# Kernel optimization log

Hardware: AMD Instinct MI355X
Metric: run time of the kernel (lower is better)

The kernel has to match this reference:

```python
import jax, jax.numpy as jnp
import numpy as np

N_NODES = 50000
N_EDGES = 800000
IN_DIM = 256
H1 = 512
H2 = 128


def _gcn_conv(x, W, b, row, col, ew, n_nodes):
    """PyG GCNConv with edge_weight: linear (no bias) -> add self-loops ->
    symmetric normalization -> weighted scatter-add -> + bias."""
    xw = x @ W  # [N, out]
    loop = jnp.arange(n_nodes, dtype=row.dtype)
    row_f = jnp.concatenate([row, loop])
    col_f = jnp.concatenate([col, loop])
    ew_f = jnp.concatenate([ew, jnp.ones((n_nodes,), dtype=ew.dtype)])
    deg = jax.ops.segment_sum(ew_f, col_f, num_segments=n_nodes)  # in-degree
    dinv = jnp.where(deg > 0, jax.lax.rsqrt(jnp.where(deg > 0, deg, 1.0)), 0.0)
    norm = dinv[row_f] * ew_f * dinv[col_f]  # [E+N]
    msg = norm[:, None] * xw[row_f]          # [E+N, out] gather
    out = jax.ops.segment_sum(msg, col_f, num_segments=n_nodes)  # scatter-add
    return out + b


def _prelu(x, alpha):
    return jnp.where(x >= 0, x, alpha * x)


def setup_inputs() -> dict:
    key = jax.random.key(0)
    ks = jax.random.split(key, 6)
    x = jax.random.normal(ks[0], (N_NODES, IN_DIM), dtype=jnp.float32)
    edge_index = jax.random.randint(ks[1], (2, N_EDGES), 0, N_NODES, dtype=jnp.int32)
    edge_attr = jax.random.uniform(ks[2], (N_EDGES,), dtype=jnp.float32)
    W1 = jax.random.normal(ks[3], (IN_DIM, H1), dtype=jnp.float32) / np.sqrt(IN_DIM)
    b1 = jnp.zeros((H1,), dtype=jnp.float32)
    W2 = jax.random.normal(ks[4], (H1, H2), dtype=jnp.float32) / np.sqrt(H1)
    b2 = jnp.zeros((H2,), dtype=jnp.float32)
    alpha = jnp.ones((1,), dtype=jnp.float32) * 0.25  # nn.PReLU default init
    return {"x": x, "edge_attr": edge_attr, "W1": W1, "b1": b1,
            "W2": W2, "b2": b2, "alpha": alpha, "edge_index": edge_index}


def reference(x, edge_attr, W1, b1, W2, b2, alpha, edge_index):
    row, col = edge_index[0], edge_index[1]
    # Dropout treated as identity (deterministic eval-mode reference).
    feat1 = _prelu(_gcn_conv(x, W1, b1, row, col, edge_attr, N_NODES), alpha)
    feat2 = _prelu(_gcn_conv(feat1, W2, b2, row, col, edge_attr, N_NODES), alpha)
    return feat2
```

## Files before the change

### kernel.cpp

```cpp
#include <hip/hip_runtime.h>

#define N_NODES 50000
#define N_EDGES 800000
#define IN_DIM  256
#define H1      512
#define H2      128

typedef __attribute__((ext_vector_type(8))) short  short8v;
typedef __attribute__((ext_vector_type(4))) float  float4v;
typedef __attribute__((ext_vector_type(4))) unsigned short ushort4v;

__device__ __forceinline__ void split_bf16(float v, unsigned short& h, unsigned short& l) {
    unsigned u = __builtin_bit_cast(unsigned, v);
    unsigned hr = (u + 0x7FFFu + ((u >> 16) & 1u)) >> 16;
    float hf = __builtin_bit_cast(float, hr << 16);
    float lf = v - hf;
    unsigned ul = __builtin_bit_cast(unsigned, lf);
    unsigned lr = (ul + 0x7FFFu + ((ul >> 16) & 1u)) >> 16;
    h = (unsigned short)hr; l = (unsigned short)lr;
}


__global__ void init_kernel(float* deg, int* cnt, int n) {
    int i = blockIdx.x * blockDim.x + threadIdx.x;
    if (i < n) { deg[i] = 1.0f; cnt[i] = 0; }
}

__global__ void edge_deg_kernel(const int* __restrict__ col, const float* __restrict__ ew,
                                float* deg, int* cnt, int ne) {
    int e = blockIdx.x * blockDim.x + threadIdx.x;
    if (e < ne) {
        int c = col[e];
        atomicAdd(&deg[c], ew[e]);
        atomicAdd(&cnt[c], 1);
    }
}

__global__ void dinv_kernel(const float* __restrict__ deg, float* dinv, int n) {
    int i = blockIdx.x * blockDim.x + threadIdx.x;
    if (i < n) dinv[i] = rsqrtf(deg[i]);
}

__global__ void scan_block_kernel(const int* __restrict__ cnt, int* __restrict__ part,
                                  int* __restrict__ bsum, int n) {
    __shared__ int s[256];
    int tid = threadIdx.x;
    int i = blockIdx.x * 256 + tid;
    int v = (i < n) ? cnt[i] : 0;
    s[tid] = v; __syncthreads();
#pragma unroll
    for (int d = 1; d < 256; d <<= 1) {
        int t = (tid >= d) ? s[tid - d] : 0; __syncthreads();
        s[tid] += t; __syncthreads();
    }
    if (i < n) part[i] = s[tid] - v;
    if (tid == 255) bsum[blockIdx.x] = s[255];
}

__global__ void scan_tops_kernel(const int* __restrict__ bsum, int* __restrict__ boff, int nb) {
    __shared__ int s[256];
    int tid = threadIdx.x;
    int v = (tid < nb) ? bsum[tid] : 0;
    s[tid] = v; __syncthreads();
#pragma unroll
    for (int d = 1; d < 256; d <<= 1) {
        int t = (tid >= d) ? s[tid - d] : 0; __syncthreads();
        s[tid] += t; __syncthreads();
    }
    if (tid < nb) boff[tid] = s[tid] - v;
}

__global__ void scan_add_kernel(const int* __restrict__ part, const int* __restrict__ boff,
                                int* __restrict__ ptr, int* __restrict__ fill, int n) {
    int i = blockIdx.x * 256 + threadIdx.x;
    if (i < n) {
        int p = part[i] + boff[blockIdx.x];
        ptr[i] = p; fill[i] = p;
    }
    if (i == 0) ptr[n] = N_EDGES;
}

__global__ void scatter_kernel(const int* __restrict__ row, const int* __restrict__ col,
                               const float* __restrict__ ew, const float* __restrict__ dinv,
                               int* fill, int2* __restrict__ edges, int ne) {
    int e = blockIdx.x * blockDim.x + threadIdx.x;
    if (e < ne) {
        int r = row[e], c = col[e];
        int pos = atomicAdd(&fill[c], 1);
        float w = dinv[r] * ew[e] * dinv[c];
        edges[pos] = make_int2(r, __float_as_int(w));
    }
}

__global__ void convw_kernel(const float* __restrict__ W, unsigned short* __restrict__ Wh,
                             unsigned short* __restrict__ Wl, int K, int N) {
    int idx = blockIdx.x * 256 + threadIdx.x;
    if (idx < N * K) {
        int n = idx / K, k = idx % K;
        unsigned short h, l;
        split_bf16(W[(size_t)k * N + n], h, l);
        Wh[idx] = h; Wl[idx] = l;
    }
}


__global__ __launch_bounds__(256) void agg256_kernel(
        const float* __restrict__ x, const float* __restrict__ dinv,
        const int* __restrict__ ptr, const int2* __restrict__ edges,
        unsigned short* __restrict__ out_h, unsigned short* __restrict__ out_l) {
    int wv = threadIdx.x >> 6, lane = threadIdx.x & 63;
    int node = blockIdx.x * 4 + wv;
    if (node >= N_NODES) return;
    const float4* x4 = (const float4*)x;
    float di = dinv[node];
    float s = di * di;
    float4 v = x4[node * 64 + lane];
    float ax = v.x * s, ay = v.y * s, az = v.z * s, aw = v.w * s;
    int j = ptr[node], e1 = ptr[node + 1];
    for (; j + 3 < e1; j += 4) {
        int2 e0 = edges[j], e1_ = edges[j + 1], e2 = edges[j + 2], e3 = edges[j + 3];
        float4 u0 = x4[e0.x * 64 + lane];
        float4 u1 = x4[e1_.x * 64 + lane];
        float4 u2 = x4[e2.x * 64 + lane];
        float4 u3 = x4[e3.x * 64 + lane];
        float c0 = __int_as_float(e0.y), c1 = __int_as_float(e1_.y);
        float c2 = __int_as_float(e2.y), c3 = __int_as_float(e3.y);
        ax += c0 * u0.x + c1 * u1.x + c2 * u2.x + c3 * u3.x;
        ay += c0 * u0.y + c1 * u1.y + c2 * u2.y + c3 * u3.y;
        az += c0 * u0.z + c1 * u1.z + c2 * u2.z + c3 * u3.z;
        aw += c0 * u0.w + c1 * u1.w + c2 * u2.w + c3 * u3.w;
    }
    for (; j < e1; ++j) {
        int2 e0 = edges[j];
        float c0 = __int_as_float(e0.y);
        float4 u0 = x4[e0.x * 64 + lane];
        ax += c0 * u0.x; ay += c0 * u0.y; az += c0 * u0.z; aw += c0 * u0.w;
    }
    unsigned short hx, lx, hy, ly, hz, lz, hw, lw;
    split_bf16(ax, hx, lx);
    split_bf16(ay, hy, ly);
    split_bf16(az, hz, lz);
    split_bf16(aw, hw, lw);
    ushort4v h4 = {hx, hy, hz, hw};
    ushort4v l4 = {lx, ly, lz, lw};
    *(ushort4v*)(out_h + (size_t)node * IN_DIM + lane * 4) = h4;
    *(ushort4v*)(out_l + (size_t)node * IN_DIM + lane * 4) = l4;
}

__global__ __launch_bounds__(256) void agg128_epi_kernel(
        const float* __restrict__ xw, const float* __restrict__ dinv,
        const int* __restrict__ ptr, const int2* __restrict__ edges,
        const float* __restrict__ b2, const float* __restrict__ alphap,
        float* __restrict__ out) {
    int wv = threadIdx.x >> 6, lane = threadIdx.x & 63;
    int node = blockIdx.x * 4 + wv;
    if (node >= N_NODES) return;
    const float2* x2 = (const float2*)xw;
    float di = dinv[node];
    float s = di * di;
    float2 v = x2[node * 64 + lane];
    float ax = v.x * s, ay = v.y * s;
    int j = ptr[node], e1 = ptr[node + 1];
    for (; j + 3 < e1; j += 4) {
        int2 e0 = edges[j], e1_ = edges[j + 1], e2 = edges[j + 2], e3 = edges[j + 3];
        float2 u0 = x2[e0.x * 64 + lane];
        float2 u1 = x2[e1_.x * 64 + lane];
        float2 u2 = x2[e2.x * 64 + lane];
        float2 u3 = x2[e3.x * 64 + lane];
        float c0 = __int_as_float(e0.y), c1 = __int_as_float(e1_.y);
        float c2 = __int_as_float(e2.y), c3 = __int_as_float(e3.y);
        ax += c0 * u0.x + c1 * u1.x + c2 * u2.x + c3 * u3.x;
        ay += c0 * u0.y + c1 * u1.y + c2 * u2.y + c3 * u3.y;
    }
    for (; j < e1; ++j) {
        int2 e0 = edges[j];
        float c0 = __int_as_float(e0.y);
        float2 u0 = x2[e0.x * 64 + lane];
        ax += c0 * u0.x; ay += c0 * u0.y;
    }
    float alpha = alphap[0];
    float2 b = ((const float2*)b2)[lane];
    ax += b.x; ay += b.y;
    ax = (ax >= 0.f) ? ax : alpha * ax;
    ay = (ay >= 0.f) ? ay : alpha * ay;
    ((float2*)out)[node * 64 + lane] = make_float2(ax, ay);
}


__device__ __forceinline__ int swz(int row, int k ) {
    return ((row << 7) + (k << 1)) ^ ((row & 7) << 4);
}

__device__ __forceinline__ void gload16(const void* g, void* l) {
    __builtin_amdgcn_global_load_lds(
        (const __attribute__((address_space(1))) unsigned int*)g,
        (__attribute__((address_space(3))) unsigned int*)l, 16, 0, 0);
}

__device__ __forceinline__ void stage_plane_async(
        const unsigned short* __restrict__ gbase,
        unsigned short* lds, int K, int grow0, int k0, int wave, int lane) {
    int r8 = lane >> 3;
    int kk = k0 + (((lane & 7) ^ r8) << 3);
#pragma unroll
    for (int t = 0; t < 4; ++t) {
        int rowblk = wave * 32 + t * 8;
        const unsigned short* g = gbase + (size_t)(grow0 + rowblk + r8) * K + kk;
        gload16(g, lds + (size_t)rowblk * 64);
    }
}

template <int MODE>
__global__ __launch_bounds__(256, 2) void gemm_mfma_kernel(
        const unsigned short* __restrict__ A_hi, const unsigned short* __restrict__ A_lo,
        const unsigned short* __restrict__ B_hi, const unsigned short* __restrict__ B_lo,
        const float* __restrict__ bias, const float* __restrict__ alphap,
        unsigned short* __restrict__ Oh, unsigned short* __restrict__ Ol,
        float* __restrict__ Of, int M, int N, int K) {
    __shared__ unsigned short smem[4][8192];
    unsigned short* Ah = smem[0];
    unsigned short* Al = smem[1];
    unsigned short* Bh = smem[2];
    unsigned short* Bl = smem[3];

    const int tid  = threadIdx.x;
    const int lane = tid & 63, wave = tid >> 6;
    const int wm = wave >> 1, wn = wave & 1;
    const int lr = lane & 15, lk = (lane >> 4) << 3;

    const int m0 = blockIdx.y * 128, n0 = blockIdx.x * 128;

    float4v acc[4][4] = {};

    for (int k0 = 0; k0 < K; k0 += 64) {
        stage_plane_async(A_hi, Ah, K, m0, k0, wave, lane);
        stage_plane_async(A_lo, Al, K, m0, k0, wave, lane);
        stage_plane_async(B_hi, Bh, K, n0, k0, wave, lane);
        stage_plane_async(B_lo, Bl, K, n0, k0, wave, lane);
        __syncthreads();
#pragma unroll
        for (int q = 0; q < 2; ++q) {
            short8v ah[4], al[4], bh[4], bl[4];
#pragma unroll
            for (int i = 0; i < 4; ++i) {
                ah[i] = *(const short8v*)((const char*)Ah + swz(wm * 64 + i * 16 + lr, q * 32 + lk));
                al[i] = *(const short8v*)((const char*)Al + swz(wm * 64 + i * 16 + lr, q * 32 + lk));
                bh[i] = *(const short8v*)((const char*)Bh + swz(wn * 64 + i * 16 + lr, q * 32 + lk));
                bl[i] = *(const short8v*)((const char*)Bl + swz(wn * 64 + i * 16 + lr, q * 32 + lk));
            }
#pragma unroll
            for (int mi = 0; mi < 4; ++mi)
#pragma unroll
                for (int ni = 0; ni < 4; ++ni) {
                    acc[mi][ni] = __builtin_amdgcn_mfma_f32_16x16x32_bf16(ah[mi], bh[ni], acc[mi][ni], 0, 0, 0);
                    acc[mi][ni] = __builtin_amdgcn_mfma_f32_16x16x32_bf16(ah[mi], bl[ni], acc[mi][ni], 0, 0, 0);
                    acc[mi][ni] = __builtin_amdgcn_mfma_f32_16x16x32_bf16(al[mi], bh[ni], acc[mi][ni], 0, 0, 0);
                }
        }
        __syncthreads();
    }

    const float alpha = (MODE == 1) ? alphap[0] : 0.f;
#pragma unroll
    for (int mi = 0; mi < 4; ++mi) {
        int grow_base = m0 + wm * 64 + mi * 16 + (lane >> 4) * 4;
#pragma unroll
        for (int ni = 0; ni < 4; ++ni) {
            int gcol = n0 + wn * 64 + ni * 16 + lr;
#pragma unroll
            for (int r = 0; r < 4; ++r) {
                int grow = grow_base + r;
                if (grow < M) {
                    float v = acc[mi][ni][r];
                    if (MODE == 1) {
                        v += bias[gcol];
                        v = (v >= 0.f) ? v : alpha * v;
                        unsigned short h, l;
                        split_bf16(v, h, l);
                        Oh[(size_t)grow * N + gcol] = h;
                        Ol[(size_t)grow * N + gcol] = l;
                    } else {
                        Of[(size_t)grow * N + gcol] = v;
                    }
                }
            }
        }
    }
}


extern "C" void kernel_launch(void* const* d_in, const int* in_sizes, int n_in,
                              void* d_out, int out_size, void* d_ws, size_t ws_size,
                              hipStream_t stream) {
    const float* x     = (const float*)d_in[0];
    const float* eattr = (const float*)d_in[1];
    const float* W1    = (const float*)d_in[2];
    const float* b1    = (const float*)d_in[3];
    const float* W2    = (const float*)d_in[4];
    const float* b2    = (const float*)d_in[5];
    const float* alpha = (const float*)d_in[6];
    const int*   eidx  = (const int*)d_in[7];
    const int* row = eidx;
    const int* col = eidx + N_EDGES;
    float* out = (float*)d_out;

    float* ws_f = (float*)d_ws;
    size_t off = 0;
    float* deg   = ws_f + off; off += N_NODES;
    float* dinv  = ws_f + off; off += N_NODES;
    int2*  edges = (int2*)(ws_f + off); off += (size_t)2 * N_EDGES;
    unsigned short* aggx_h = (unsigned short*)(ws_f + off); off += (size_t)N_NODES * IN_DIM / 2;
    unsigned short* aggx_l = (unsigned short*)(ws_f + off); off += (size_t)N_NODES * IN_DIM / 2;
    float* xw2 = (float*)aggx_h;
    unsigned short* feat1_h = (unsigned short*)(ws_f + off); off += (size_t)N_NODES * H1 / 2;
    unsigned short* feat1_l = (unsigned short*)(ws_f + off); off += (size_t)N_NODES * H1 / 2;
    unsigned short* W1t_h = (unsigned short*)(ws_f + off); off += (size_t)IN_DIM * H1 / 2;
    unsigned short* W1t_l = (unsigned short*)(ws_f + off); off += (size_t)IN_DIM * H1 / 2;
    unsigned short* W2t_h = (unsigned short*)(ws_f + off); off += (size_t)H1 * H2 / 2;
    unsigned short* W2t_l = (unsigned short*)(ws_f + off); off += (size_t)H1 * H2 / 2;
    int* cnt  = (int*)(ws_f + off); off += N_NODES;
    int* ptr  = (int*)(ws_f + off); off += N_NODES + 1;
    int* fill = (int*)(ws_f + off); off += N_NODES;
    int* part = (int*)(ws_f + off); off += N_NODES;
    int* bsum = (int*)(ws_f + off); off += 256;
    int* boff = (int*)(ws_f + off); off += 256;

    const int nodeBlocks = (N_NODES + 255) / 256;
    const int edgeBlocks = (N_EDGES + 255) / 256;

    convw_kernel<<<(IN_DIM * H1 + 255) / 256, 256, 0, stream>>>(W1, W1t_h, W1t_l, IN_DIM, H1);
    convw_kernel<<<(H1 * H2 + 255) / 256, 256, 0, stream>>>(W2, W2t_h, W2t_l, H1, H2);

    init_kernel<<<nodeBlocks, 256, 0, stream>>>(deg, cnt, N_NODES);
    edge_deg_kernel<<<edgeBlocks, 256, 0, stream>>>(col, eattr, deg, cnt, N_EDGES);
    dinv_kernel<<<nodeBlocks, 256, 0, stream>>>(deg, dinv, N_NODES);
    scan_block_kernel<<<nodeBlocks, 256, 0, stream>>>(cnt, part, bsum, N_NODES);
    scan_tops_kernel<<<1, 256, 0, stream>>>(bsum, boff, nodeBlocks);
    scan_add_kernel<<<nodeBlocks, 256, 0, stream>>>(part, boff, ptr, fill, N_NODES);
    scatter_kernel<<<edgeBlocks, 256, 0, stream>>>(row, col, eattr, dinv, fill, edges, N_EDGES);

    agg256_kernel<<<(N_NODES + 3) / 4, 256, 0, stream>>>(x, dinv, ptr, edges, aggx_h, aggx_l);
    {
        dim3 grid(H1 / 128, (N_NODES + 127) / 128);
        gemm_mfma_kernel<1><<<grid, 256, 0, stream>>>(aggx_h, aggx_l, W1t_h, W1t_l,
                                                      b1, alpha, feat1_h, feat1_l, nullptr,
                                                      N_NODES, H1, IN_DIM);
    }

    {
        dim3 grid(H2 / 128, (N_NODES + 127) / 128);
        gemm_mfma_kernel<0><<<grid, 256, 0, stream>>>(feat1_h, feat1_l, W2t_h, W2t_l,
                                                      nullptr, nullptr, nullptr, nullptr, xw2,
                                                      N_NODES, H2, H1);
    }
    agg128_epi_kernel<<<(N_NODES + 3) / 4, 256, 0, stream>>>(xw2, dinv, ptr, edges, b2, alpha, out);
}
```

Measured before the change: 525.2 us.

## Split layer-1 aggregation into column halves, remap GEMM tiles per XCD, prefetch next K tile

The 256-wide gather aggregation now runs as two launches, each covering 128 columns. This halves the gathered working set per pass so it has a better chance of staying in cache. The GEMM switches to a 1D grid with an XCD-aware remap, so consecutive tiles land on the same XCD and share L2. The GEMM loop also loads LDS fragments into registers and issues the async stage of the next K tile before running the MFMAs, overlapping the load with compute. The costs are an extra launch, re-reading the edge list, and higher register pressure from the doubled fragment arrays.

```diff
diff --git a/kernel.cpp b/kernel.cpp
--- a/kernel.cpp
+++ b/kernel.cpp
@@ -8,7 +8,6 @@
 
 typedef __attribute__((ext_vector_type(8))) short  short8v;
 typedef __attribute__((ext_vector_type(4))) float  float4v;
-typedef __attribute__((ext_vector_type(4))) unsigned short ushort4v;
 
 __device__ __forceinline__ void split_bf16(float v, unsigned short& h, unsigned short& l) {
     unsigned u = __builtin_bit_cast(unsigned, v);
@@ -104,47 +103,42 @@
 }
 
 
-__global__ __launch_bounds__(256) void agg256_kernel(
+__global__ __launch_bounds__(256) void agg256_half_kernel(
         const float* __restrict__ x, const float* __restrict__ dinv,
         const int* __restrict__ ptr, const int2* __restrict__ edges,
-        unsigned short* __restrict__ out_h, unsigned short* __restrict__ out_l) {
+        unsigned short* __restrict__ out_h, unsigned short* __restrict__ out_l, int d0) {
     int wv = threadIdx.x >> 6, lane = threadIdx.x & 63;
     int node = blockIdx.x * 4 + wv;
     if (node >= N_NODES) return;
-    const float4* x4 = (const float4*)x;
+    const float* xb = x + d0 + lane * 2;
     float di = dinv[node];
     float s = di * di;
-    float4 v = x4[node * 64 + lane];
-    float ax = v.x * s, ay = v.y * s, az = v.z * s, aw = v.w * s;
+    float2 v = *(const float2*)(xb + (size_t)node * IN_DIM);
+    float ax = v.x * s, ay = v.y * s;
     int j = ptr[node], e1 = ptr[node + 1];
     for (; j + 3 < e1; j += 4) {
         int2 e0 = edges[j], e1_ = edges[j + 1], e2 = edges[j + 2], e3 = edges[j + 3];
-        float4 u0 = x4[e0.x * 64 + lane];
-        float4 u1 = x4[e1_.x * 64 + lane];
-        float4 u2 = x4[e2.x * 64 + lane];
-        float4 u3 = x4[e3.x * 64 + lane];
+        float2 u0 = *(const float2*)(xb + (size_t)e0.x * IN_DIM);
+        float2 u1 = *(const float2*)(xb + (size_t)e1_.x * IN_DIM);
+        float2 u2 = *(const float2*)(xb + (size_t)e2.x * IN_DIM);
+        float2 u3 = *(const float2*)(xb + (size_t)e3.x * IN_DIM);
         float c0 = __int_as_float(e0.y), c1 = __int_as_float(e1_.y);
         float c2 = __int_as_float(e2.y), c3 = __int_as_float(e3.y);
         ax += c0 * u0.x + c1 * u1.x + c2 * u2.x + c3 * u3.x;
         ay += c0 * u0.y + c1 * u1.y + c2 * u2.y + c3 * u3.y;
-        az += c0 * u0.z + c1 * u1.z + c2 * u2.z + c3 * u3.z;
-        aw += c0 * u0.w + c1 * u1.w + c2 * u2.w + c3 * u3.w;
     }
     for (; j < e1; ++j) {
         int2 e0 = edges[j];
         float c0 = __int_as_float(e0.y);
-        float4 u0 = x4[e0.x * 64 + lane];
-        ax += c0 * u0.x; ay += c0 * u0.y; az += c0 * u0.z; aw += c0 * u0.w;
-    }
-    unsigned short hx, lx, hy, ly, hz, lz, hw, lw;
-    split_bf16(ax, hx, lx);
-    split_bf16(ay, hy, ly);
-    split_bf16(az, hz, lz);
-    split_bf16(aw, hw, lw);
-    ushort4v h4 = {hx, hy, hz, hw};
-    ushort4v l4 = {lx, ly, lz, lw};
-    *(ushort4v*)(out_h + (size_t)node * IN_DIM + lane * 4) = h4;
-    *(ushort4v*)(out_l + (size_t)node * IN_DIM + lane * 4) = l4;
+        float2 u0 = *(const float2*)(xb + (size_t)e0.x * IN_DIM);
+        ax += c0 * u0.x; ay += c0 * u0.y;
+    }
+    unsigned short h0, l0, h1, l1;
+    split_bf16(ax, h0, l0);
+    split_bf16(ay, h1, l1);
+    size_t o = (size_t)node * IN_DIM + d0;
+    ((unsigned*)(out_h + o))[lane] = (unsigned)h0 | ((unsigned)h1 << 16);
+    ((unsigned*)(out_l + o))[lane] = (unsigned)l0 | ((unsigned)l1 << 16);
 }
 
 __global__ __launch_bounds__(256) void agg128_epi_kernel(
@@ -216,7 +210,7 @@
         const unsigned short* __restrict__ B_hi, const unsigned short* __restrict__ B_lo,
         const float* __restrict__ bias, const float* __restrict__ alphap,
         unsigned short* __restrict__ Oh, unsigned short* __restrict__ Ol,
-        float* __restrict__ Of, int M, int N, int K) {
+        float* __restrict__ Of, int M, int N, int K, int tilesX) {
     __shared__ unsigned short smem[4][8192];
     unsigned short* Ah = smem[0];
     unsigned short* Al = smem[1];
@@ -228,36 +222,48 @@
     const int wm = wave >> 1, wn = wave & 1;
     const int lr = lane & 15, lk = (lane >> 4) << 3;
 
-    const int m0 = blockIdx.y * 128, n0 = blockIdx.x * 128;
+    const int nwg = gridDim.x;
+    const int q_ = nwg >> 3, r_ = nwg & 7;
+    const int xcd = blockIdx.x & 7, idx = blockIdx.x >> 3;
+    const int wg = ((xcd < r_) ? xcd * (q_ + 1) : r_ * (q_ + 1) + (xcd - r_) * q_) + idx;
+    const int m0 = (wg / tilesX) * 128, n0 = (wg % tilesX) * 128;
 
     float4v acc[4][4] = {};
 
+    stage_plane_async(A_hi, Ah, K, m0, 0, wave, lane);
+    stage_plane_async(A_lo, Al, K, m0, 0, wave, lane);
+    stage_plane_async(B_hi, Bh, K, n0, 0, wave, lane);
+    stage_plane_async(B_lo, Bl, K, n0, 0, wave, lane);
+
     for (int k0 = 0; k0 < K; k0 += 64) {
-        stage_plane_async(A_hi, Ah, K, m0, k0, wave, lane);
-        stage_plane_async(A_lo, Al, K, m0, k0, wave, lane);
-        stage_plane_async(B_hi, Bh, K, n0, k0, wave, lane);
-        stage_plane_async(B_lo, Bl, K, n0, k0, wave, lane);
         __syncthreads();
-#pragma unroll
-        for (int q = 0; q < 2; ++q) {
-            short8v ah[4], al[4], bh[4], bl[4];
+        short8v ah[2][4], al[2][4], bh[2][4], bl[2][4];
+#pragma unroll
+        for (int q = 0; q < 2; ++q)
 #pragma unroll
             for (int i = 0; i < 4; ++i) {
-                ah[i] = *(const short8v*)((const char*)Ah + swz(wm * 64 + i * 16 + lr, q * 32 + lk));
-                al[i] = *(const short8v*)((const char*)Al + swz(wm * 64 + i * 16 + lr, q * 32 + lk));
-                bh[i] = *(const short8v*)((const char*)Bh + swz(wn * 64 + i * 16 + lr, q * 32 + lk));
-                bl[i] = *(const short8v*)((const char*)Bl + swz(wn * 64 + i * 16 + lr, q * 32 + lk));
+                ah[q][i] = *(const short8v*)((const char*)Ah + swz(wm * 64 + i * 16 + lr, q * 32 + lk));
+                al[q][i] = *(const short8v*)((const char*)Al + swz(wm * 64 + i * 16 + lr, q * 32 + lk));
+                bh[q][i] = *(const short8v*)((const char*)Bh + swz(wn * 64 + i * 16 + lr, q * 32 + lk));
+                bl[q][i] = *(const short8v*)((const char*)Bl + swz(wn * 64 + i * 16 + lr, q * 32 + lk));
             }
+        __syncthreads();
+        if (k0 + 64 < K) {
+            stage_plane_async(A_hi, Ah, K, m0, k0 + 64, wave, lane);
+            stage_plane_async(A_lo, Al, K, m0, k0 + 64, wave, lane);
+            stage_plane_async(B_hi, Bh, K, n0, k0 + 64, wave, lane);
+            stage_plane_async(B_lo, Bl, K, n0, k0 + 64, wave, lane);
+        }
+#pragma unroll
+        for (int q = 0; q < 2; ++q)
 #pragma unroll
             for (int mi = 0; mi < 4; ++mi)
 #pragma unroll
                 for (int ni = 0; ni < 4; ++ni) {
-                    acc[mi][ni] = __builtin_amdgcn_mfma_f32_16x16x32_bf16(ah[mi], bh[ni], acc[mi][ni], 0, 0, 0);
-                    acc[mi][ni] = __builtin_amdgcn_mfma_f32_16x16x32_bf16(ah[mi], bl[ni], acc[mi][ni], 0, 0, 0);
-                    acc[mi][ni] = __builtin_amdgcn_mfma_f32_16x16x32_bf16(al[mi], bh[ni], acc[mi][ni], 0, 0, 0);
+                    acc[mi][ni] = __builtin_amdgcn_mfma_f32_16x16x32_bf16(ah[q][mi], bh[q][ni], acc[mi][ni], 0, 0, 0);
+                    acc[mi][ni] = __builtin_amdgcn_mfma_f32_16x16x32_bf16(ah[q][mi], bl[q][ni], acc[mi][ni], 0, 0, 0);
+                    acc[mi][ni] = __builtin_amdgcn_mfma_f32_16x16x32_bf16(al[q][mi], bh[q][ni], acc[mi][ni], 0, 0, 0);
                 }
-        }
-        __syncthreads();
     }
 
     const float alpha = (MODE == 1) ? alphap[0] : 0.f;
@@ -339,19 +345,20 @@
     scan_add_kernel<<<nodeBlocks, 256, 0, stream>>>(part, boff, ptr, fill, N_NODES);
     scatter_kernel<<<edgeBlocks, 256, 0, stream>>>(row, col, eattr, dinv, fill, edges, N_EDGES);
 
-    agg256_kernel<<<(N_NODES + 3) / 4, 256, 0, stream>>>(x, dinv, ptr, edges, aggx_h, aggx_l);
+    agg256_half_kernel<<<(N_NODES + 3) / 4, 256, 0, stream>>>(x, dinv, ptr, edges, aggx_h, aggx_l, 0);
+    agg256_half_kernel<<<(N_NODES + 3) / 4, 256, 0, stream>>>(x, dinv, ptr, edges, aggx_h, aggx_l, 128);
     {
-        dim3 grid(H1 / 128, (N_NODES + 127) / 128);
-        gemm_mfma_kernel<1><<<grid, 256, 0, stream>>>(aggx_h, aggx_l, W1t_h, W1t_l,
-                                                      b1, alpha, feat1_h, feat1_l, nullptr,
-                                                      N_NODES, H1, IN_DIM);
+        int tilesX = H1 / 128, tilesY = (N_NODES + 127) / 128;
+        gemm_mfma_kernel<1><<<tilesX * tilesY, 256, 0, stream>>>(
+            aggx_h, aggx_l, W1t_h, W1t_l, b1, alpha, feat1_h, feat1_l, nullptr,
+            N_NODES, H1, IN_DIM, tilesX);
     }
 
     {
-        dim3 grid(H2 / 128, (N_NODES + 127) / 128);
-        gemm_mfma_kernel<0><<<grid, 256, 0, stream>>>(feat1_h, feat1_l, W2t_h, W2t_l,
-                                                      nullptr, nullptr, nullptr, nullptr, xw2,
-                                                      N_NODES, H2, H1);
+        int tilesX = H2 / 128, tilesY = (N_NODES + 127) / 128;
+        gemm_mfma_kernel<0><<<tilesX * tilesY, 256, 0, stream>>>(
+            feat1_h, feat1_l, W2t_h, W2t_l, nullptr, nullptr, nullptr, nullptr, xw2,
+            N_NODES, H2, H1, tilesX);
     }
     agg128_epi_kernel<<<(N_NODES + 3) / 4, 256, 0, stream>>>(xw2, dinv, ptr, edges, b2, alpha, out);
 }
```

Result: no change. 519.1 us (-1.2%).
